# Kernel optimization log

Measured on AMD Instinct MI355X. Metric: run time of the kernel, lower is better.

Reference implementation:

```python
import jax, jax.numpy as jnp
import numpy as np

B, HH, WW, C = 1, 96, 96, 128
HEADS, K = 4, 7

def setup_inputs() -> dict:
    key = jax.random.key(0)
    ks = jax.random.split(key, 6)
    def lin(k, o, i):
        return jax.random.normal(k, (o, i), jnp.float32) * (1.0 / np.sqrt(i))
    return {
        "x": jax.random.normal(ks[0], (B, HH, WW, C), jnp.float32),
        "qkv_w": lin(ks[1], 3 * C, C),
        "qkv_b": jnp.zeros((3 * C,), jnp.float32),
        "proj_w": lin(ks[2], C, C),
        "proj_b": jnp.zeros((C,), jnp.float32),
        "fc1_w": lin(ks[3], 4 * C, C),
        "fc1_b": jnp.zeros((4 * C,), jnp.float32),
        "fc2_w": lin(ks[4], C, 4 * C),
        "fc2_b": jnp.zeros((C,), jnp.float32),
    }

def _na2d(q, k, v):
    # q,k,v: [B, heads, H, W, hd]; NATTEN 2D neighborhood attention,
    # kernel K, stride 1, dilation 1, non-causal. Windows are clamped at
    # borders so each query attends to exactly K*K in-bounds keys.
    Bq, h, Hs, Ws, hd = q.shape
    start_h = jnp.clip(jnp.arange(Hs) - K // 2, 0, Hs - K)
    idx_h = start_h[:, None] + jnp.arange(K)  # [H, K]
    start_w = jnp.clip(jnp.arange(Ws) - K // 2, 0, Ws - K)
    idx_w = start_w[:, None] + jnp.arange(K)  # [W, K]
    I = idx_h[:, None, :, None]  # -> [H, W, K, K] broadcast
    J = idx_w[None, :, None, :]
    k_nb = k[:, :, I, J, :]  # [B, heads, H, W, K, K, hd]
    v_nb = v[:, :, I, J, :]
    scale = jnp.asarray(hd, q.dtype) ** -0.5
    logits = jnp.einsum('bhijd,bhijkld->bhijkl', q, k_nb) * scale
    attn = jax.nn.softmax(logits.reshape(Bq, h, Hs, Ws, K * K), axis=-1)
    attn = attn.reshape(Bq, h, Hs, Ws, K, K)
    return jnp.einsum('bhijkl,bhijkld->bhijd', attn, v_nb)

def reference(x, qkv_w, qkv_b, proj_w, proj_b, fc1_w, fc1_b, fc2_w, fc2_b):
    Bq, Hs, Ws, Cc = x.shape
    hd = Cc // HEADS
    qkv = x @ qkv_w.T + qkv_b  # [B,H,W,3C]
    q, k, v = jnp.split(qkv, 3, axis=-1)
    def to_heads(t):
        return t.reshape(Bq, Hs, Ws, HEADS, hd).transpose(0, 3, 1, 2, 4)
    o = _na2d(to_heads(q), to_heads(k), to_heads(v))  # [B,heads,H,W,hd]
    o = o.transpose(0, 2, 3, 1, 4).reshape(Bq, Hs, Ws, Cc)
    x0 = o @ proj_w.T + proj_b
    h1 = jax.nn.gelu(x0 @ fc1_w.T + fc1_b, approximate=False)
    return h1 @ fc2_w.T + fc2_b
```

## Files before the change

### kernel.cpp

```cpp
#include <hip/hip_runtime.h>

typedef __bf16 bf16_t;
typedef __bf16 bf16x8 __attribute__((ext_vector_type(8)));
typedef __bf16 bf16x4 __attribute__((ext_vector_type(4)));
typedef float f32x4 __attribute__((ext_vector_type(4)));
typedef int   i32x4 __attribute__((ext_vector_type(4)));

#define HH 96
#define WW 96
#define CC 128
#define HD 32
#define TOK (HH * WW)
#define PLANE (TOK * CC)
#define KW 7

#define W_QKV  0
#define W_PROJ 49152
#define W_FC1  65536
#define W_FC2  131072
#define W_TOT  196608

#define PATCH 10
#define PSZ 100
#define NPAD 112
#define STR 136
#define H1S 520

#define L_P    0
#define L_OS   8704
#define L_X0   10880
#define L_VOFF 13056
#define L_TOT  13312

__device__ __forceinline__ bf16x8 cvt8(const float* __restrict__ p) {
    const f32x4 a = *(const f32x4*)p;
    const f32x4 b = *(const f32x4*)(p + 4);
    bf16x8 r;
    r[0] = (bf16_t)a[0]; r[1] = (bf16_t)a[1]; r[2] = (bf16_t)a[2]; r[3] = (bf16_t)a[3];
    r[4] = (bf16_t)b[0]; r[5] = (bf16_t)b[1]; r[6] = (bf16_t)b[2]; r[7] = (bf16_t)b[3];
    return r;
}

template <int NT>
__device__ __forceinline__ void mmaN(const bf16_t* __restrict__ A, int lda,
                                     const bf16_t* __restrict__ W, int ldb,
                                     int K, f32x4* acc) {
    const int lane = threadIdx.x & 63;
    const bf16_t* ap = A + (lane & 15) * lda + ((lane >> 4) * 8);
    const bf16_t* bp = W + (lane & 15) * ldb + ((lane >> 4) * 8);
    for (int k0 = 0; k0 < K; k0 += 32) {
        bf16x8 a = *(const bf16x8*)(ap + k0);
#pragma unroll
        for (int t = 0; t < NT; t++) {
            bf16x8 b = *(const bf16x8*)(bp + t * 16 * ldb + k0);
            acc[t] = __builtin_amdgcn_mfma_f32_16x16x32_bf16(a, b, acc[t], 0, 0, 0);
        }
    }
}

__global__ __launch_bounds__(256) void k_prep(const float* __restrict__ x,
                                              const float* __restrict__ qkv_w,
                                              const float* __restrict__ proj_w,
                                              const float* __restrict__ fc1_w,
                                              const float* __restrict__ fc2_w,
                                              bf16_t* __restrict__ xb,
                                              bf16_t* __restrict__ wb) {
    const int idx = blockIdx.x * 256 + threadIdx.x;
    const int NX = PLANE / 4;
    const float* src;
    bf16_t* dst;
    int base;
    if (idx < NX) {
        base = idx * 4; src = x + base; dst = xb + base;
    } else {
        base = (idx - NX) * 4;
        if (base >= W_TOT) return;
        dst = wb + base;
        if (base < W_PROJ)     src = qkv_w  + base;
        else if (base < W_FC1) src = proj_w + (base - W_PROJ);
        else if (base < W_FC2) src = fc1_w  + (base - W_FC1);
        else                   src = fc2_w  + (base - W_FC2);
    }
    const f32x4 a = *(const f32x4*)src;
    bf16x4 r;
    r[0] = (bf16_t)a[0]; r[1] = (bf16_t)a[1]; r[2] = (bf16_t)a[2]; r[3] = (bf16_t)a[3];
    *(bf16x4*)dst = r;
}

__global__ __launch_bounds__(256) void k_qkv(const bf16_t* __restrict__ xb,
                                             const bf16_t* __restrict__ wb,
                                             const float* __restrict__ bias,
                                             bf16_t* __restrict__ qb,
                                             bf16_t* __restrict__ kb,
                                             bf16_t* __restrict__ vb) {
    const int wid = blockIdx.x * 4 + (threadIdx.x >> 6);
    const int m0 = (wid / 6) * 16;
    const int n0 = (wid % 6) * 64;
    const int lane = threadIdx.x & 63;
    const int g = lane >> 4, li = lane & 15;
    f32x4 acc[4] = {};
    mmaN<4>(xb + m0 * CC, CC, wb + W_QKV + n0 * CC, CC, CC, acc);
#pragma unroll
    for (int t = 0; t < 4; t++) {
        const int n = n0 + t * 16 + li;
        const float bb = bias[n];
        const int part = n >> 7, c = n & 127;
        bf16_t* dst = (part == 0) ? qb : (part == 1) ? kb : vb;
#pragma unroll
        for (int r = 0; r < 4; r++)
            dst[(m0 + g * 4 + r) * CC + c] = (bf16_t)(acc[t][r] + bb);
    }
}

__global__ __launch_bounds__(256, 3) void k_attn_mlp(
        const bf16_t* __restrict__ qb, const bf16_t* __restrict__ kg,
        const bf16_t* __restrict__ vg, const bf16_t* __restrict__ wb,
        const float* __restrict__ proj_b, const float* __restrict__ fc1_b,
        const float* __restrict__ fc2_b,  float* __restrict__ out) {
    __shared__ __align__(16) bf16_t smem[L_TOT];
    bf16_t* Pbuf = smem + L_P;
    bf16_t* o_s  = smem + L_OS;
    bf16_t* x0s  = smem + L_X0;
    bf16_t* h1s  = smem + L_P;
    int*    voff = (int*)(smem + L_VOFF);

    const int tid = threadIdx.x;
    const int w = tid >> 6, lane = tid & 63;
    const int g = lane >> 4, li = lane & 15;
    const int bid = blockIdx.x;
    const int i0 = (bid / 24) * 4, j0 = (bid % 24) * 4;
    const int pr0 = min(max(i0 - 3, 0), HH - PATCH);
    const int pc0 = min(max(j0 - 3, 0), WW - PATCH);
    const int ch = w * HD;

    if (tid < 128) {
        const int p = min(tid, PSZ - 1);
        const int pi = p / 10, pj = p - 10 * pi;
        voff[tid] = ((pr0 + pi) * WW + pc0 + pj) * CC;
    }
    __syncthreads();

    f32x4 lg[7];
    {
        const int qi = i0 + (li >> 2), qj = j0 + (li & 3);
        const bf16x8 aq = *(const bf16x8*)(qb + (qi * WW + qj) * CC + ch + g * 8);
#pragma unroll
        for (int t = 0; t < 7; t++) {
            const bf16x8 bk = *(const bf16x8*)(kg + voff[t * 16 + li] + ch + g * 8);
            lg[t] = __builtin_amdgcn_mfma_f32_16x16x32_bf16(aq, bk, (f32x4){0.f,0.f,0.f,0.f}, 0, 0, 0);
        }
    }
    int lr[4], lc[4];
#pragma unroll
    for (int r = 0; r < 4; r++) {
        const int m = g * 4 + r;
        const int i = i0 + (m >> 2), j = j0 + (m & 3);
        lr[r] = min(max(i - 3, 0), HH - KW) - pr0;
        lc[r] = min(max(j - 3, 0), WW - KW) - pc0;
    }
    const float scale = 0.17677669529663687f;
#pragma unroll
    for (int t = 0; t < 7; t++) {
        const int col = t * 16 + li;
        const int pi = col / 10, pj = col - 10 * pi;
#pragma unroll
        for (int r = 0; r < 4; r++) {
            const bool valid = (col < PSZ) &&
                               ((unsigned)(pi - lr[r]) <= 6u) &&
                               ((unsigned)(pj - lc[r]) <= 6u);
            lg[t][r] = valid ? lg[t][r] * scale : -1e30f;
        }
    }
    f32x4 mx = lg[0], sm;
#pragma unroll
    for (int t = 1; t < 7; t++)
#pragma unroll
        for (int r = 0; r < 4; r++) mx[r] = fmaxf(mx[r], lg[t][r]);
#pragma unroll
    for (int off = 8; off; off >>= 1)
#pragma unroll
        for (int r = 0; r < 4; r++) mx[r] = fmaxf(mx[r], __shfl_xor(mx[r], off));
#pragma unroll
    for (int r = 0; r < 4; r++) sm[r] = 0.f;
#pragma unroll
    for (int t = 0; t < 7; t++)
#pragma unroll
        for (int r = 0; r < 4; r++) {
            lg[t][r] = __expf(lg[t][r] - mx[r]);
            sm[r] += lg[t][r];
        }
#pragma unroll
    for (int off = 8; off; off >>= 1)
#pragma unroll
        for (int r = 0; r < 4; r++) sm[r] += __shfl_xor(sm[r], off);
#pragma unroll
    for (int r = 0; r < 4; r++) sm[r] = 1.f / sm[r];

    bf16_t* Pw = Pbuf + w * 16 * STR;
#pragma unroll
    for (int t = 0; t < 7; t++)
#pragma unroll
        for (int r = 0; r < 4; r++)
            Pw[(g * 4 + r) * STR + t * 16 + li] = (bf16_t)(lg[t][r] * sm[r]);
    *(bf16x4*)(Pw + (lane >> 2) * STR + NPAD + (lane & 3) * 4) = (bf16x4){0,0,0,0};

    f32x4 oA[2] = {};
#pragma unroll
    for (int ks0 = 0; ks0 < 128; ks0 += 32) {
        const bf16x8 a = *(const bf16x8*)(Pw + li * STR + ks0 + g * 8);
        const i32x4 o0 = *(const i32x4*)&voff[ks0 + g * 8];
        const i32x4 o1 = *(const i32x4*)&voff[ks0 + g * 8 + 4];
#pragma unroll
        for (int t2 = 0; t2 < 2; t2++) {
            const int cb = ch + t2 * 16 + li;
            bf16x8 b;
            b[0] = vg[o0[0] + cb]; b[1] = vg[o0[1] + cb];
            b[2] = vg[o0[2] + cb]; b[3] = vg[o0[3] + cb];
            b[4] = vg[o1[0] + cb]; b[5] = vg[o1[1] + cb];
            b[6] = vg[o1[2] + cb]; b[7] = vg[o1[3] + cb];
            oA[t2] = __builtin_amdgcn_mfma_f32_16x16x32_bf16(a, b, oA[t2], 0, 0, 0);
        }
    }
#pragma unroll
    for (int t2 = 0; t2 < 2; t2++)
#pragma unroll
        for (int r = 0; r < 4; r++)
            o_s[(g * 4 + r) * STR + ch + t2 * 16 + li] = (bf16_t)oA[t2][r];
    __syncthreads();

    {
        f32x4 acc[2] = {};
        mmaN<2>(o_s, STR, wb + W_PROJ + (w * 32) * CC, CC, CC, acc);
#pragma unroll
        for (int t = 0; t < 2; t++) {
            const int n = w * 32 + t * 16 + li;
            const float bb = proj_b[n];
#pragma unroll
            for (int r = 0; r < 4; r++)
                x0s[(g * 4 + r) * STR + n] = (bf16_t)(acc[t][r] + bb);
        }
    }
    __syncthreads();

    {
        f32x4 acc[8] = {};
        mmaN<8>(x0s, STR, wb + W_FC1 + (w * 128) * CC, CC, CC, acc);
#pragma unroll
        for (int t = 0; t < 8; t++) {
            const int n = w * 128 + t * 16 + li;
            const float bb = fc1_b[n];
#pragma unroll
            for (int r = 0; r < 4; r++) {
                const int m = g * 4 + r;
                const float xv = acc[t][r] + bb;
                const float u = 0.7978845608028654f * (xv + 0.044715f * xv * xv * xv);
                const float e = __expf(2.f * u);
                const float gg = 0.5f * xv * (2.f - 2.f / (e + 1.f));
                h1s[m * H1S + n] = (bf16_t)gg;
            }
        }
    }
    __syncthreads();

    {
        f32x4 acc[2] = {};
        mmaN<2>(h1s, H1S, wb + W_FC2 + (w * 32) * (4 * CC), 4 * CC, 4 * CC, acc);
#pragma unroll
        for (int t = 0; t < 2; t++) {
            const int n = w * 32 + t * 16 + li;
            const float bb = fc2_b[n];
#pragma unroll
            for (int r = 0; r < 4; r++) {
                const int m = g * 4 + r;
                const int i = i0 + (m >> 2), j = j0 + (m & 3);
                float xv = acc[t][r] + bb;
                xv = fminf(fmaxf(xv, -1e4f), 1e4f);
                out[(i * WW + j) * CC + n] = xv;
            }
        }
    }
}

extern "C" void kernel_launch(void* const* d_in, const int* in_sizes, int n_in,
                              void* d_out, int out_size, void* d_ws, size_t ws_size,
                              hipStream_t stream) {
    const float* x      = (const float*)d_in[0];
    const float* qkv_w  = (const float*)d_in[1];
    const float* qkv_b  = (const float*)d_in[2];
    const float* proj_w = (const float*)d_in[3];
    const float* proj_b = (const float*)d_in[4];
    const float* fc1_w  = (const float*)d_in[5];
    const float* fc1_b  = (const float*)d_in[6];
    const float* fc2_w  = (const float*)d_in[7];
    const float* fc2_b  = (const float*)d_in[8];

    bf16_t* ws = (bf16_t*)d_ws;
    bf16_t* wb = ws;
    bf16_t* xb = ws + W_TOT;
    bf16_t* qb = xb + PLANE;
    bf16_t* kb = qb + PLANE;
    bf16_t* vb = kb + PLANE;
    float* out = (float*)d_out;

    k_prep    <<<1344, 256, 0, stream>>>(x, qkv_w, proj_w, fc1_w, fc2_w, xb, wb);
    k_qkv     <<<864,  256, 0, stream>>>(xb, wb, qkv_b, qb, kb, vb);
    k_attn_mlp<<<576,  256, 0, stream>>>(qb, kb, vb, wb,
                                         proj_b, fc1_b, fc2_b, out);
}
```

Measured before the change: 118.4 us.

## Store V transposed and use a rectangular 10x16 key patch for vector loads

The QKV kernel now writes V channel-major, transposing each 16-token tile through LDS. The attention kernel can then fetch eight consecutive V tokens with one vector load instead of eight scalar gathers through an offset table. The key/value patch becomes a rectangular 10x16 window, so token addresses are computed arithmetically and the voff LDS table and its barrier are removed. In exchange the logits and PV MFMAs grow from 7 to 10 tiles and K from 128 to 160, with more masked work.

```diff
diff --git a/kernel.cpp b/kernel.cpp
--- a/kernel.cpp
+++ b/kernel.cpp
@@ -2,9 +2,9 @@
 
 typedef __bf16 bf16_t;
 typedef __bf16 bf16x8 __attribute__((ext_vector_type(8)));
+typedef bf16x8 bf16x8u __attribute__((aligned(8)));
 typedef __bf16 bf16x4 __attribute__((ext_vector_type(4)));
 typedef float f32x4 __attribute__((ext_vector_type(4)));
-typedef int   i32x4 __attribute__((ext_vector_type(4)));
 
 #define HH 96
 #define WW 96
@@ -21,16 +21,16 @@
 #define W_TOT  196608
 
 #define PATCH 10
-#define PSZ 100
-#define NPAD 112
+#define PCW 16
+#define PK 160
+#define PSTR 168
 #define STR 136
 #define H1S 520
 
 #define L_P    0
-#define L_OS   8704
-#define L_X0   10880
-#define L_VOFF 13056
-#define L_TOT  13312
+#define L_OS   10752
+#define L_X0   12928
+#define L_TOT  15104
 
 __device__ __forceinline__ bf16x8 cvt8(const float* __restrict__ p) {
     const f32x4 a = *(const f32x4*)p;
@@ -92,7 +92,8 @@
                                              const float* __restrict__ bias,
                                              bf16_t* __restrict__ qb,
                                              bf16_t* __restrict__ kb,
-                                             bf16_t* __restrict__ vb) {
+                                             bf16_t* __restrict__ vt) {
+    __shared__ __align__(16) bf16_t vtile[2 * 64 * 24];
     const int wid = blockIdx.x * 4 + (threadIdx.x >> 6);
     const int m0 = (wid / 6) * 16;
     const int n0 = (wid % 6) * 64;
@@ -100,21 +101,40 @@
     const int g = lane >> 4, li = lane & 15;
     f32x4 acc[4] = {};
     mmaN<4>(xb + m0 * CC, CC, wb + W_QKV + n0 * CC, CC, CC, acc);
-#pragma unroll
-    for (int t = 0; t < 4; t++) {
-        const int n = n0 + t * 16 + li;
-        const float bb = bias[n];
-        const int part = n >> 7, c = n & 127;
-        bf16_t* dst = (part == 0) ? qb : (part == 1) ? kb : vb;
-#pragma unroll
-        for (int r = 0; r < 4; r++)
-            dst[(m0 + g * 4 + r) * CC + c] = (bf16_t)(acc[t][r] + bb);
+    if (n0 < 256) {
+#pragma unroll
+        for (int t = 0; t < 4; t++) {
+            const int n = n0 + t * 16 + li;
+            const float bb = bias[n];
+            const int c = n & 127;
+            bf16_t* dst = (n >> 7) ? kb : qb;
+#pragma unroll
+            for (int r = 0; r < 4; r++)
+                dst[(m0 + g * 4 + r) * CC + c] = (bf16_t)(acc[t][r] + bb);
+        }
+    } else {
+        const int cw = n0 - 256;
+        bf16_t* tile = vtile + (cw >> 6) * (64 * 24);
+#pragma unroll
+        for (int t = 0; t < 4; t++) {
+            const int n = n0 + t * 16 + li;
+            const float bb = bias[n];
+#pragma unroll
+            for (int r = 0; r < 4; r++)
+                tile[(t * 16 + li) * 24 + g * 4 + r] = (bf16_t)(acc[t][r] + bb);
+        }
+        asm volatile("s_waitcnt lgkmcnt(0)" ::: "memory");
+        const bf16x8 u0 = *(const bf16x8*)(tile + lane * 24);
+        const bf16x8 u1 = *(const bf16x8*)(tile + lane * 24 + 8);
+        bf16_t* dst = vt + (cw + lane) * TOK + m0;
+        *(bf16x8*)dst = u0;
+        *(bf16x8*)(dst + 8) = u1;
     }
 }
 
 __global__ __launch_bounds__(256, 3) void k_attn_mlp(
         const bf16_t* __restrict__ qb, const bf16_t* __restrict__ kg,
-        const bf16_t* __restrict__ vg, const bf16_t* __restrict__ wb,
+        const bf16_t* __restrict__ vt, const bf16_t* __restrict__ wb,
         const float* __restrict__ proj_b, const float* __restrict__ fc1_b,
         const float* __restrict__ fc2_b,  float* __restrict__ out) {
     __shared__ __align__(16) bf16_t smem[L_TOT];
@@ -122,7 +142,6 @@
     bf16_t* o_s  = smem + L_OS;
     bf16_t* x0s  = smem + L_X0;
     bf16_t* h1s  = smem + L_P;
-    int*    voff = (int*)(smem + L_VOFF);
 
     const int tid = threadIdx.x;
     const int w = tid >> 6, lane = tid & 63;
@@ -130,23 +149,17 @@
     const int bid = blockIdx.x;
     const int i0 = (bid / 24) * 4, j0 = (bid % 24) * 4;
     const int pr0 = min(max(i0 - 3, 0), HH - PATCH);
-    const int pc0 = min(max(j0 - 3, 0), WW - PATCH);
+    const int pc0 = min(max(j0 - 4, 0), WW - PCW);
     const int ch = w * HD;
 
-    if (tid < 128) {
-        const int p = min(tid, PSZ - 1);
-        const int pi = p / 10, pj = p - 10 * pi;
-        voff[tid] = ((pr0 + pi) * WW + pc0 + pj) * CC;
-    }
-    __syncthreads();
-
-    f32x4 lg[7];
+    f32x4 lg[10];
     {
         const int qi = i0 + (li >> 2), qj = j0 + (li & 3);
         const bf16x8 aq = *(const bf16x8*)(qb + (qi * WW + qj) * CC + ch + g * 8);
 #pragma unroll
-        for (int t = 0; t < 7; t++) {
-            const bf16x8 bk = *(const bf16x8*)(kg + voff[t * 16 + li] + ch + g * 8);
+        for (int t = 0; t < 10; t++) {
+            const int tok = (pr0 + t) * WW + pc0 + li;
+            const bf16x8 bk = *(const bf16x8*)(kg + tok * CC + ch + g * 8);
             lg[t] = __builtin_amdgcn_mfma_f32_16x16x32_bf16(aq, bk, (f32x4){0.f,0.f,0.f,0.f}, 0, 0, 0);
         }
     }
@@ -160,20 +173,17 @@
     }
     const float scale = 0.17677669529663687f;
 #pragma unroll
-    for (int t = 0; t < 7; t++) {
-        const int col = t * 16 + li;
-        const int pi = col / 10, pj = col - 10 * pi;
+    for (int t = 0; t < 10; t++) {
 #pragma unroll
         for (int r = 0; r < 4; r++) {
-            const bool valid = (col < PSZ) &&
-                               ((unsigned)(pi - lr[r]) <= 6u) &&
-                               ((unsigned)(pj - lc[r]) <= 6u);
+            const bool valid = ((unsigned)(t - lr[r]) <= 6u) &&
+                               ((unsigned)(li - lc[r]) <= 6u);
             lg[t][r] = valid ? lg[t][r] * scale : -1e30f;
         }
     }
     f32x4 mx = lg[0], sm;
 #pragma unroll
-    for (int t = 1; t < 7; t++)
+    for (int t = 1; t < 10; t++)
 #pragma unroll
         for (int r = 0; r < 4; r++) mx[r] = fmaxf(mx[r], lg[t][r]);
 #pragma unroll
@@ -183,7 +193,7 @@
 #pragma unroll
     for (int r = 0; r < 4; r++) sm[r] = 0.f;
 #pragma unroll
-    for (int t = 0; t < 7; t++)
+    for (int t = 0; t < 10; t++)
 #pragma unroll
         for (int r = 0; r < 4; r++) {
             lg[t][r] = __expf(lg[t][r] - mx[r]);
@@ -196,28 +206,23 @@
 #pragma unroll
     for (int r = 0; r < 4; r++) sm[r] = 1.f / sm[r];
 
-    bf16_t* Pw = Pbuf + w * 16 * STR;
-#pragma unroll
-    for (int t = 0; t < 7; t++)
+    bf16_t* Pw = Pbuf + w * 16 * PSTR;
+#pragma unroll
+    for (int t = 0; t < 10; t++)
 #pragma unroll
         for (int r = 0; r < 4; r++)
-            Pw[(g * 4 + r) * STR + t * 16 + li] = (bf16_t)(lg[t][r] * sm[r]);
-    *(bf16x4*)(Pw + (lane >> 2) * STR + NPAD + (lane & 3) * 4) = (bf16x4){0,0,0,0};
+            Pw[(g * 4 + r) * PSTR + t * 16 + li] = (bf16_t)(lg[t][r] * sm[r]);
 
     f32x4 oA[2] = {};
 #pragma unroll
-    for (int ks0 = 0; ks0 < 128; ks0 += 32) {
-        const bf16x8 a = *(const bf16x8*)(Pw + li * STR + ks0 + g * 8);
-        const i32x4 o0 = *(const i32x4*)&voff[ks0 + g * 8];
-        const i32x4 o1 = *(const i32x4*)&voff[ks0 + g * 8 + 4];
+    for (int ks0 = 0; ks0 < PK; ks0 += 32) {
+        const int kb_ = ks0 + g * 8;
+        const int tokb = (pr0 + (kb_ >> 4)) * WW + pc0 + (kb_ & 15);
+        const bf16x8 a = *(const bf16x8*)(Pw + li * PSTR + ks0 + g * 8);
 #pragma unroll
         for (int t2 = 0; t2 < 2; t2++) {
             const int cb = ch + t2 * 16 + li;
-            bf16x8 b;
-            b[0] = vg[o0[0] + cb]; b[1] = vg[o0[1] + cb];
-            b[2] = vg[o0[2] + cb]; b[3] = vg[o0[3] + cb];
-            b[4] = vg[o1[0] + cb]; b[5] = vg[o1[1] + cb];
-            b[6] = vg[o1[2] + cb]; b[7] = vg[o1[3] + cb];
+            const bf16x8 b = *(const bf16x8u*)(vt + cb * TOK + tokb);
             oA[t2] = __builtin_amdgcn_mfma_f32_16x16x32_bf16(a, b, oA[t2], 0, 0, 0);
         }
     }
@@ -299,11 +304,11 @@
     bf16_t* xb = ws + W_TOT;
     bf16_t* qb = xb + PLANE;
     bf16_t* kb = qb + PLANE;
-    bf16_t* vb = kb + PLANE;
+    bf16_t* vt = kb + PLANE;
     float* out = (float*)d_out;
 
     k_prep    <<<1344, 256, 0, stream>>>(x, qkv_w, proj_w, fc1_w, fc2_w, xb, wb);
-    k_qkv     <<<864,  256, 0, stream>>>(xb, wb, qkv_b, qb, kb, vb);
-    k_attn_mlp<<<576,  256, 0, stream>>>(qb, kb, vb, wb,
+    k_qkv     <<<864,  256, 0, stream>>>(xb, wb, qkv_b, qb, kb, vt);
+    k_attn_mlp<<<576,  256, 0, stream>>>(qb, kb, vt, wb,
                                          proj_b, fc1_b, fc2_b, out);
 }
```

Result: slower. 124.5 us (+5.1%).

## Fuse fp32-to-bf16 conversion into QKV GEMM and drop the prep kernel

Applied to the files above, without the earlier changes.

Removes the separate prep kernel. The QKV projection now loads fp32 x and qkv_w directly and converts them to bf16 in registers before the MFMA. Extra blocks in the same launch convert the proj/fc1/fc2 weights for the later attention+MLP kernel. This saves one launch and the write-then-read round trip of the bf16 copy of x, at the cost of fp32 global loads (twice the bytes) inside the GEMM inner loop.

```diff
diff --git a/kernel.cpp b/kernel.cpp
--- a/kernel.cpp
+++ b/kernel.cpp
@@ -32,7 +32,7 @@
 #define L_VOFF 13056
 #define L_TOT  13312
 
-__device__ __forceinline__ bf16x8 cvt8(const float* __restrict__ p) {
+__device__ __forceinline__ bf16x8 ld8f(const float* __restrict__ p) {
     const f32x4 a = *(const f32x4*)p;
     const f32x4 b = *(const f32x4*)(p + 4);
     bf16x8 r;
@@ -58,48 +58,57 @@
     }
 }
 
-__global__ __launch_bounds__(256) void k_prep(const float* __restrict__ x,
+__global__ __launch_bounds__(256) void k_qkv2(const float* __restrict__ x,
                                               const float* __restrict__ qkv_w,
                                               const float* __restrict__ proj_w,
                                               const float* __restrict__ fc1_w,
                                               const float* __restrict__ fc2_w,
-                                              bf16_t* __restrict__ xb,
+                                              const float* __restrict__ bias,
+                                              bf16_t* __restrict__ qb,
+                                              bf16_t* __restrict__ kb,
+                                              bf16_t* __restrict__ vb,
                                               bf16_t* __restrict__ wb) {
-    const int idx = blockIdx.x * 256 + threadIdx.x;
-    const int NX = PLANE / 4;
-    const float* src;
-    bf16_t* dst;
-    int base;
-    if (idx < NX) {
-        base = idx * 4; src = x + base; dst = xb + base;
-    } else {
-        base = (idx - NX) * 4;
-        if (base >= W_TOT) return;
-        dst = wb + base;
-        if (base < W_PROJ)     src = qkv_w  + base;
-        else if (base < W_FC1) src = proj_w + (base - W_PROJ);
-        else if (base < W_FC2) src = fc1_w  + (base - W_FC1);
-        else                   src = fc2_w  + (base - W_FC2);
-    }
-    const f32x4 a = *(const f32x4*)src;
-    bf16x4 r;
-    r[0] = (bf16_t)a[0]; r[1] = (bf16_t)a[1]; r[2] = (bf16_t)a[2]; r[3] = (bf16_t)a[3];
-    *(bf16x4*)dst = r;
-}
-
-__global__ __launch_bounds__(256) void k_qkv(const bf16_t* __restrict__ xb,
-                                             const bf16_t* __restrict__ wb,
-                                             const float* __restrict__ bias,
-                                             bf16_t* __restrict__ qb,
-                                             bf16_t* __restrict__ kb,
-                                             bf16_t* __restrict__ vb) {
-    const int wid = blockIdx.x * 4 + (threadIdx.x >> 6);
+    const int nb = blockIdx.x;
+    const int tid = threadIdx.x;
+
+    if (nb >= 864) {
+        const int idx0 = (nb - 864) * 256 + tid;
+#pragma unroll
+        for (int r = 0; r < 3; r++) {
+            const int base = W_PROJ + (idx0 + r * 12288) * 4;
+            const float* src;
+            if (base < W_FC1)      src = proj_w + (base - W_PROJ);
+            else if (base < W_FC2) src = fc1_w  + (base - W_FC1);
+            else                   src = fc2_w  + (base - W_FC2);
+            const f32x4 a = *(const f32x4*)src;
+            bf16x4 rv;
+            rv[0] = (bf16_t)a[0]; rv[1] = (bf16_t)a[1];
+            rv[2] = (bf16_t)a[2]; rv[3] = (bf16_t)a[3];
+            *(bf16x4*)(wb + base) = rv;
+        }
+        return;
+    }
+
+    const int wid = nb * 4 + (tid >> 6);
     const int m0 = (wid / 6) * 16;
     const int n0 = (wid % 6) * 64;
-    const int lane = threadIdx.x & 63;
+    const int lane = tid & 63;
     const int g = lane >> 4, li = lane & 15;
+
     f32x4 acc[4] = {};
-    mmaN<4>(xb + m0 * CC, CC, wb + W_QKV + n0 * CC, CC, CC, acc);
+    {
+        const float* ap = x + (m0 + li) * CC + g * 8;
+        const float* bp = qkv_w + (n0 + li) * CC + g * 8;
+#pragma unroll
+        for (int k0 = 0; k0 < CC; k0 += 32) {
+            const bf16x8 a = ld8f(ap + k0);
+#pragma unroll
+            for (int t = 0; t < 4; t++) {
+                const bf16x8 b = ld8f(bp + t * 16 * CC + k0);
+                acc[t] = __builtin_amdgcn_mfma_f32_16x16x32_bf16(a, b, acc[t], 0, 0, 0);
+            }
+        }
+    }
 #pragma unroll
     for (int t = 0; t < 4; t++) {
         const int n = n0 + t * 16 + li;
@@ -296,14 +305,13 @@
 
     bf16_t* ws = (bf16_t*)d_ws;
     bf16_t* wb = ws;
-    bf16_t* xb = ws + W_TOT;
-    bf16_t* qb = xb + PLANE;
+    bf16_t* qb = ws + W_TOT;
     bf16_t* kb = qb + PLANE;
     bf16_t* vb = kb + PLANE;
     float* out = (float*)d_out;
 
-    k_prep    <<<1344, 256, 0, stream>>>(x, qkv_w, proj_w, fc1_w, fc2_w, xb, wb);
-    k_qkv     <<<864,  256, 0, stream>>>(xb, wb, qkv_b, qb, kb, vb);
-    k_attn_mlp<<<576,  256, 0, stream>>>(qb, kb, vb, wb,
-                                         proj_b, fc1_b, fc2_b, out);
-}
+    k_qkv2    <<<912, 256, 0, stream>>>(x, qkv_w, proj_w, fc1_w, fc2_w,
+                                        qkv_b, qb, kb, vb, wb);
+    k_attn_mlp<<<576, 256, 0, stream>>>(qb, kb, vb, wb,
+                                        proj_b, fc1_b, fc2_b, out);
+}
```

Measured after the change: 123.3 us. 4.1% more time.
